# Kernel optimization log

Measured on AMD Instinct MI355X. Metric: run time of the kernel, lower is better.

The kernel has to match this reference:

```python
import jax, jax.numpy as jnp
import numpy as np

B, T, D = 4, 2048, 1024
H, HD = 16, 64  # num_heads, head_size; H*HD == D
DFF = 4 * D
EPS = 1e-5

def _ln(x, g, b):
    mu = jnp.mean(x, axis=-1, keepdims=True)
    var = jnp.mean(jnp.square(x - mu), axis=-1, keepdims=True)
    return (x - mu) * jax.lax.rsqrt(var + EPS) * g + b

def setup_inputs() -> dict:
    key = jax.random.key(0)
    ks = jax.random.split(key, 12)
    s = lambda fan_in: 1.0 / np.sqrt(fan_in)
    return {
        "x": jax.random.normal(ks[0], (B, T, D), jnp.float32),
        "Wq": jax.random.normal(ks[1], (H, D, HD), jnp.float32) * s(D),
        "Wk": jax.random.normal(ks[2], (H, D, HD), jnp.float32) * s(D),
        "Wv": jax.random.normal(ks[3], (H, D, HD), jnp.float32) * s(D),
        "Wo": jax.random.normal(ks[4], (D, D), jnp.float32) * s(D),
        "bo": jax.random.normal(ks[5], (D,), jnp.float32) * 0.01,
        "W1": jax.random.normal(ks[6], (D, DFF), jnp.float32) * s(D),
        "b1": jax.random.normal(ks[7], (DFF,), jnp.float32) * 0.01,
        "W2": jax.random.normal(ks[8], (DFF, D), jnp.float32) * s(DFF),
        "b2": jax.random.normal(ks[9], (D,), jnp.float32) * 0.01,
        "g1": jnp.ones((D,), jnp.float32),
        "be1": jnp.zeros((D,), jnp.float32),
        "g2": jnp.ones((D,), jnp.float32),
        "be2": jnp.zeros((D,), jnp.float32),
    }

def reference(x, Wq, Wk, Wv, Wo, bo, W1, b1, W2, b2, g1, be1, g2, be2):
    # pre-LN attention
    h = _ln(x, g1, be1)                                   # [B,T,D]
    q = jnp.einsum('btd,hde->bhte', h, Wq)                # [B,H,T,HD]
    k = jnp.einsum('btd,hde->bhte', h, Wk)
    v = jnp.einsum('btd,hde->bhte', h, Wv)
    scores = jnp.einsum('bhte,bhse->bhts', q, k) * (HD ** -0.5)  # [B,H,T,T]
    mask = jnp.tril(jnp.ones((T, T), bool))
    scores = jnp.where(mask, scores, -jnp.inf)
    attn = jax.nn.softmax(scores, axis=-1)
    ctx = jnp.einsum('bhts,bhse->bhte', attn, v)          # [B,H,T,HD]
    ctx = ctx.transpose(0, 2, 1, 3).reshape(B, T, D)      # concat heads
    x = x + jnp.einsum('btd,de->bte', ctx, Wo) + bo
    # pre-LN FFN
    h2 = _ln(x, g2, be2)
    ff = jax.nn.relu(jnp.einsum('btd,df->btf', h2, W1) + b1)
    x = x + jnp.einsum('btf,fd->btd', ff, W2) + b2
    return x
```

## Files before the change

kernel.cpp:

```cpp
#include <hip/hip_runtime.h>
#include <stdint.h>

#define B_ 4
#define T_ 2048
#define D_ 1024
#define H_ 16
#define HD_ 64
#define DFF_ 4096
#define M_ (B_ * T_)

typedef __bf16 bf16x8 __attribute__((ext_vector_type(8)));
typedef float f32x4 __attribute__((ext_vector_type(4)));

__device__ __forceinline__ uint16_t f2bf(float f) {
  union { float f; uint32_t u; } v;
  v.f = f;
  uint32_t r = v.u + 0x7FFF + ((v.u >> 16) & 1);
  return (uint16_t)(r >> 16);
}

#define GLD_LDS(gp, lp)                                                        \
  __builtin_amdgcn_global_load_lds(                                            \
      (const __attribute__((address_space(1))) void*)(gp),                     \
      (__attribute__((address_space(3))) void*)(lp), 16, 0, 0)

__global__ __launch_bounds__(256) void ln_bf16(const float* __restrict__ x,
                                               const float* __restrict__ gamma,
                                               const float* __restrict__ beta,
                                               uint16_t* __restrict__ out) {
  __shared__ float red[4];
  const int tid = threadIdx.x;
  const size_t row = blockIdx.x;
  const float4 v = ((const float4*)(x + row * D_))[tid];
  float s = v.x + v.y + v.z + v.w;
#pragma unroll
  for (int off = 32; off >= 1; off >>= 1) s += __shfl_xor(s, off, 64);
  if ((tid & 63) == 0) red[tid >> 6] = s;
  __syncthreads();
  const float mean = (red[0] + red[1] + red[2] + red[3]) * (1.0f / D_);
  const float d0 = v.x - mean, d1 = v.y - mean, d2 = v.z - mean, d3 = v.w - mean;
  float ss = d0 * d0 + d1 * d1 + d2 * d2 + d3 * d3;
#pragma unroll
  for (int off = 32; off >= 1; off >>= 1) ss += __shfl_xor(ss, off, 64);
  __syncthreads();
  if ((tid & 63) == 0) red[tid >> 6] = ss;
  __syncthreads();
  const float var = (red[0] + red[1] + red[2] + red[3]) * (1.0f / D_);
  const float rstd = rsqrtf(var + 1e-5f);
  const float4 g = ((const float4*)gamma)[tid];
  const float4 b = ((const float4*)beta)[tid];
  ushort4 o;
  o.x = f2bf(d0 * rstd * g.x + b.x);
  o.y = f2bf(d1 * rstd * g.y + b.y);
  o.z = f2bf(d2 * rstd * g.z + b.z);
  o.w = f2bf(d3 * rstd * g.w + b.w);
  ((ushort4*)(out + row * D_))[tid] = o;
}

__global__ __launch_bounds__(256) void transpose_cast(const float* __restrict__ in,
                                                      uint16_t* __restrict__ out,
                                                      int R, int C) {
  __shared__ float tile[32][33];
  const int tx = threadIdx.x & 31, ty = threadIdx.x >> 5;
  const int c0 = blockIdx.x * 32, r0 = blockIdx.y * 32;
#pragma unroll
  for (int i = 0; i < 32; i += 8)
    tile[ty + i][tx] = in[(size_t)(r0 + ty + i) * C + c0 + tx];
  __syncthreads();
#pragma unroll
  for (int i = 0; i < 32; i += 8)
    out[(size_t)(c0 + ty + i) * R + r0 + tx] = f2bf(tile[tx][ty + i]);
}

__global__ __launch_bounds__(256) void qkv_wt(const float* __restrict__ Wq,
                                              const float* __restrict__ Wk,
                                              const float* __restrict__ Wv,
                                              uint16_t* __restrict__ out) {
  __shared__ float tile[32][33];
  const int tx = threadIdx.x & 31, ty = threadIdx.x >> 5;
  const int z = blockIdx.z, which = z >> 4, hh = z & 15;
  const float* W = (which == 0) ? Wq : ((which == 1) ? Wk : Wv);
  const float* in = W + (size_t)hh * D_ * HD_;
  const int e0 = blockIdx.x * 32, d0 = blockIdx.y * 32;
#pragma unroll
  for (int i = 0; i < 32; i += 8)
    tile[ty + i][tx] = in[(size_t)(d0 + ty + i) * HD_ + e0 + tx];
  __syncthreads();
#pragma unroll
  for (int i = 0; i < 32; i += 8)
    out[((size_t)(which * 1024 + hh * 64) + e0 + ty + i) * D_ + d0 + tx] =
        f2bf(tile[tx][ty + i]);
}

__global__ __launch_bounds__(256) void gemm_bf16(const uint16_t* __restrict__ A,
                                                 const uint16_t* __restrict__ Bt,
                                                 void* __restrict__ C,
                                                 const float* __restrict__ bias,
                                                 const float* __restrict__ resid,
                                                 int M, int N, int K, int flags) {
  __shared__ __align__(16) uint16_t As[128 * 32];
  __shared__ __align__(16) uint16_t Bs[128 * 32];
  const int tid = threadIdx.x;
  const int lane = tid & 63, w = tid >> 6;
  const int quad = lane >> 4, lr = lane & 15;
  const int wr = w >> 1, wc = w & 1;
  const int bn0 = blockIdx.x * 128, bm0 = blockIdx.y * 128;

  f32x4 acc[4][4];
#pragma unroll
  for (int i = 0; i < 4; i++)
#pragma unroll
    for (int j = 0; j < 4; j++) acc[i][j] = f32x4{0.f, 0.f, 0.f, 0.f};

  const int s_sub = lane >> 2, s_slot = lane & 3;

  for (int k0 = 0; k0 < K; k0 += 32) {
#pragma unroll
    for (int i = 0; i < 2; i++) {
      const int r = w * 32 + i * 16 + s_sub;
      const int cg = s_slot ^ ((r >> 1) & 3);
      GLD_LDS(A + (size_t)(bm0 + r) * K + k0 + cg * 8, As + (w * 32 + i * 16) * 32);
      GLD_LDS(Bt + (size_t)(bn0 + r) * K + k0 + cg * 8, Bs + (w * 32 + i * 16) * 32);
    }
    __syncthreads();

    bf16x8 af[4], bfr[4];
#pragma unroll
    for (int i = 0; i < 4; i++) {
      const int m = wr * 64 + i * 16 + lr;
      const int slot = quad ^ ((m >> 1) & 3);
      af[i] = *(const bf16x8*)(As + m * 32 + slot * 8);
    }
#pragma unroll
    for (int j = 0; j < 4; j++) {
      const int n = wc * 64 + j * 16 + lr;
      const int slot = quad ^ ((n >> 1) & 3);
      bfr[j] = *(const bf16x8*)(Bs + n * 32 + slot * 8);
    }
#pragma unroll
    for (int i = 0; i < 4; i++)
#pragma unroll
      for (int j = 0; j < 4; j++)
        acc[i][j] = __builtin_amdgcn_mfma_f32_16x16x32_bf16(af[i], bfr[j], acc[i][j], 0, 0, 0);
    __syncthreads();
  }

  const int base_m = bm0 + wr * 64 + quad * 4;
  const int base_n = bn0 + wc * 64 + lr;
#pragma unroll
  for (int i = 0; i < 4; i++) {
#pragma unroll
    for (int j = 0; j < 4; j++) {
      const int col = base_n + j * 16;
      const float bv = bias ? bias[col] : 0.f;
#pragma unroll
      for (int r = 0; r < 4; r++) {
        const size_t row = base_m + i * 16 + r;
        float v = acc[i][j][r] + bv;
        if (resid) v += resid[row * N + col];
        if (flags & 1) v = fmaxf(v, 0.f);
        if (flags & 2)
          ((uint16_t*)C)[row * N + col] = f2bf(v);
        else
          ((float*)C)[row * N + col] = v;
      }
    }
  }
}

__global__ __launch_bounds__(256) void v_transpose(const uint16_t* __restrict__ qkv,
                                                   uint16_t* __restrict__ vtb) {
  __shared__ __align__(16) uint16_t tile[64 * 72];
  const int tid = threadIdx.x;
  const int t0 = blockIdx.x * 64;
  const int bh = blockIdx.y;
  const int b = bh >> 4, h = bh & 15;
  const uint16_t* src = qkv + (size_t)b * T_ * 3072 + 2048 + h * 64;
#pragma unroll
  for (int u = 0; u < 2; u++) {
    const int uu = tid + u * 256;
    const int r = uu >> 3, c = uu & 7;
    *(int4*)(tile + r * 72 + c * 8) =
        *(const int4*)(src + (size_t)(t0 + r) * 3072 + c * 8);
  }
  __syncthreads();
  uint16_t* dst = vtb + ((size_t)bh * 64) * T_ + t0;
#pragma unroll
  for (int u = 0; u < 2; u++) {
    const int uu = tid + u * 256;
    const int e = uu >> 3, c2 = uu & 7;
    union { uint16_t u16[8]; int4 v; } tmp;
#pragma unroll
    for (int jj = 0; jj < 8; jj++) tmp.u16[jj] = tile[(c2 * 8 + jj) * 72 + e];
    *(int4*)(dst + (size_t)e * T_ + c2 * 8) = tmp.v;
  }
}

__global__ __launch_bounds__(256) void attn_mfma(const uint16_t* __restrict__ qkv,
                                                 const uint16_t* __restrict__ vtb,
                                                 uint16_t* __restrict__ ctx) {
  __shared__ __align__(16) uint16_t Ks[64 * 72];
  __shared__ __align__(16) uint16_t Vt[64 * 72];
  __shared__ __align__(16) uint16_t Ps[128 * 72];
  const int tid = threadIdx.x;
  const int lane = tid & 63, w = tid >> 6;
  const int quad = lane >> 4, lr = lane & 15;
  const int h = blockIdx.y, b = blockIdx.z;
  const uint16_t* base = qkv + (size_t)b * T_ * 3072 + h * 64;
  const uint16_t* vbase = vtb + ((size_t)(b * H_ + h) * 64) * T_;
  const int sr = tid >> 3, sc = tid & 7;

#pragma unroll
  for (int half = 0; half < 2; half++) {
    const int tq = (half == 0) ? (int)blockIdx.x : 15 - (int)blockIdx.x;
    const int q0 = tq * 128;

    bf16x8 aq[2][2];
#pragma unroll
    for (int i = 0; i < 2; i++)
#pragma unroll
      for (int ks = 0; ks < 2; ks++)
        aq[i][ks] = *(const bf16x8*)(base + (size_t)(q0 + w * 32 + i * 16 + lr) * 3072 +
                                     ks * 32 + quad * 8);

    f32x4 oacc[2][4];
#pragma unroll
    for (int i = 0; i < 2; i++)
#pragma unroll
      for (int j = 0; j < 4; j++) oacc[i][j] = f32x4{0.f, 0.f, 0.f, 0.f};
    float l_part[2] = {0.f, 0.f};

    const int row_min_w = q0 + w * 32;
    const int row_max_w = row_min_w + 31;
    const int nt = 2 * tq + 2;

    for (int st = 0; st < nt; st++) {
      __syncthreads();
#pragma unroll
      for (int u = 0; u < 2; u++) {
        const int r = sr + u * 32;
        *(int4*)(Ks + r * 72 + sc * 8) =
            *(const int4*)(base + 1024 + (size_t)(st * 64 + r) * 3072 + sc * 8);
        *(int4*)(Vt + r * 72 + sc * 8) =
            *(const int4*)(vbase + (size_t)r * T_ + st * 64 + sc * 8);
      }
      __syncthreads();

      if (st * 64 > row_max_w) continue;

      f32x4 sa[2][4];
#pragma unroll
      for (int i = 0; i < 2; i++)
#pragma unroll
        for (int sf = 0; sf < 4; sf++) sa[i][sf] = f32x4{0.f, 0.f, 0.f, 0.f};
#pragma unroll
      for (int ks = 0; ks < 2; ks++) {
        bf16x8 ak[4];
#pragma unroll
        for (int sf = 0; sf < 4; sf++)
          ak[sf] = *(const bf16x8*)(Ks + (sf * 16 + lr) * 72 + ks * 32 + quad * 8);
#pragma unroll
        for (int i = 0; i < 2; i++)
#pragma unroll
          for (int sf = 0; sf < 4; sf++)
            sa[i][sf] = __builtin_amdgcn_mfma_f32_16x16x32_bf16(ak[sf], aq[i][ks],
                                                                sa[i][sf], 0, 0, 0);
      }

#pragma unroll
      for (int i = 0; i < 2; i++) {
        const int mrow = q0 + w * 32 + i * 16 + lr;
#pragma unroll
        for (int sf = 0; sf < 4; sf++) {
          const int s0 = st * 64 + sf * 16 + quad * 4;
          float p[4];
#pragma unroll
          for (int r = 0; r < 4; r++) {
            float sv = sa[i][sf][r];
            if (s0 + r > mrow) sv = -1e30f;
            p[r] = exp2f(fmaf(sv, 0.18033688f, -28.8539008f));
            l_part[i] += p[r];
          }
          ushort4 pk;
          pk.x = f2bf(p[0]);
          pk.y = f2bf(p[1]);
          pk.z = f2bf(p[2]);
          pk.w = f2bf(p[3]);
          *(ushort4*)(Ps + (size_t)(w * 32 + i * 16 + lr) * 72 + sf * 16 + quad * 4) = pk;
        }
      }

#pragma unroll
      for (int ks = 0; ks < 2; ks++) {
        bf16x8 ap[2], bv[4];
#pragma unroll
        for (int i = 0; i < 2; i++)
          ap[i] = *(const bf16x8*)(Ps + (size_t)(w * 32 + i * 16 + lr) * 72 + ks * 32 +
                                   quad * 8);
#pragma unroll
        for (int j = 0; j < 4; j++)
          bv[j] = *(const bf16x8*)(Vt + (j * 16 + lr) * 72 + ks * 32 + quad * 8);
#pragma unroll
        for (int i = 0; i < 2; i++)
#pragma unroll
          for (int j = 0; j < 4; j++)
            oacc[i][j] =
                __builtin_amdgcn_mfma_f32_16x16x32_bf16(ap[i], bv[j], oacc[i][j], 0, 0, 0);
      }
    }

    float linv[2];
#pragma unroll
    for (int i = 0; i < 2; i++) {
      float l = l_part[i];
      l += __shfl_xor(l, 16, 64);
      l += __shfl_xor(l, 32, 64);
      linv[i] = 1.f / l;
    }
    uint16_t* ob =
        ctx + ((size_t)b * T_ + q0 + w * 32 + quad * 4) * D_ + h * 64 + lr;
#pragma unroll
    for (int i = 0; i < 2; i++)
#pragma unroll
      for (int r = 0; r < 4; r++) {
        const float inv = __shfl(linv[i], quad * 4 + r, 64);
#pragma unroll
        for (int j = 0; j < 4; j++)
          ob[(size_t)(i * 16 + r) * D_ + j * 16] = f2bf(oacc[i][j][r] * inv);
      }
  }
}

extern "C" void kernel_launch(void* const* d_in, const int* in_sizes, int n_in,
                              void* d_out, int out_size, void* d_ws, size_t ws_size,
                              hipStream_t stream) {
  const float* x = (const float*)d_in[0];
  const float* Wq = (const float*)d_in[1];
  const float* Wk = (const float*)d_in[2];
  const float* Wv = (const float*)d_in[3];
  const float* Wo = (const float*)d_in[4];
  const float* bo = (const float*)d_in[5];
  const float* W1 = (const float*)d_in[6];
  const float* b1 = (const float*)d_in[7];
  const float* W2 = (const float*)d_in[8];
  const float* b2 = (const float*)d_in[9];
  const float* g1 = (const float*)d_in[10];
  const float* be1 = (const float*)d_in[11];
  const float* g2 = (const float*)d_in[12];
  const float* be2 = (const float*)d_in[13];
  float* out = (float*)d_out;

  const size_t MB = 1024ull * 1024ull;
  if (ws_size < 200 * MB) return;
  char* ws = (char*)d_ws;
  uint16_t* hbuf = (uint16_t*)(ws + 0 * MB);
  uint16_t* wqkvt = (uint16_t*)(ws + 16 * MB);
  uint16_t* wot = (uint16_t*)(ws + 22 * MB);
  uint16_t* w1t = (uint16_t*)(ws + 24 * MB);
  uint16_t* w2t = (uint16_t*)(ws + 32 * MB);
  float* x1 = (float*)(ws + 40 * MB);
  uint16_t* qkvb = (uint16_t*)(ws + 72 * MB);
  uint16_t* ctxb = (uint16_t*)(ws + 120 * MB);
  uint16_t* vtb = (uint16_t*)(ws + 136 * MB);
  uint16_t* ffb = (uint16_t*)(ws + 136 * MB);

  qkv_wt<<<dim3(2, 32, 48), 256, 0, stream>>>(Wq, Wk, Wv, wqkvt);
  transpose_cast<<<dim3(32, 32), 256, 0, stream>>>(Wo, wot, 1024, 1024);
  transpose_cast<<<dim3(128, 32), 256, 0, stream>>>(W1, w1t, 1024, 4096);
  transpose_cast<<<dim3(32, 128), 256, 0, stream>>>(W2, w2t, 4096, 1024);

  ln_bf16<<<M_, 256, 0, stream>>>(x, g1, be1, hbuf);
  gemm_bf16<<<dim3(24, 64), 256, 0, stream>>>(hbuf, wqkvt, qkvb, nullptr, nullptr,
                                              M_, 3 * D_, D_, 2);
  v_transpose<<<dim3(T_ / 64, B_ * H_), 256, 0, stream>>>(qkvb, vtb);
  attn_mfma<<<dim3(8, H_, B_), 256, 0, stream>>>(qkvb, vtb, ctxb);
  gemm_bf16<<<dim3(8, 64), 256, 0, stream>>>(ctxb, wot, x1, bo, x, M_, D_, D_, 0);
  ln_bf16<<<M_, 256, 0, stream>>>(x1, g2, be2, hbuf);
  gemm_bf16<<<dim3(32, 64), 256, 0, stream>>>(hbuf, w1t, ffb, b1, nullptr, M_, DFF_,
                                              D_, 1 | 2);
  gemm_bf16<<<dim3(8, 64), 256, 0, stream>>>(ffb, w2t, out, b2, x1, M_, D_, DFF_, 0);
}
```

Before: 629.2 us.

## Add grouped tile rasterization to GEMM and split-K the FFN2 projection

The GEMM now takes a 1D grid and maps block ids so that groups of 16 M-tiles sweep across N, aiming to improve L2 reuse of weight and activation tiles. Explicit leading dimensions are added so the second FFN GEMM can be split along K into two half-GEMMs writing fp32 partials. A new elementwise kernel sums the partials with the bias and residual. The split adds extra partial-sum memory traffic and a launch, and the two halves still run one after the other.

```diff
diff --git a/kernel.cpp b/kernel.cpp
--- a/kernel.cpp
+++ b/kernel.cpp
@@ -97,14 +97,23 @@
                                                  void* __restrict__ C,
                                                  const float* __restrict__ bias,
                                                  const float* __restrict__ resid,
-                                                 int M, int N, int K, int flags) {
+                                                 int M, int N, int K, int lda,
+                                                 int ldb, int flags) {
   __shared__ __align__(16) uint16_t As[128 * 32];
   __shared__ __align__(16) uint16_t Bs[128 * 32];
   const int tid = threadIdx.x;
   const int lane = tid & 63, w = tid >> 6;
   const int quad = lane >> 4, lr = lane & 15;
   const int wr = w >> 1, wc = w & 1;
-  const int bn0 = blockIdx.x * 128, bm0 = blockIdx.y * 128;
+
+  const int n_tiles = N >> 7;
+  const int pid = blockIdx.x;
+  const int grp = 16 * n_tiles;
+  const int gid = pid / grp;
+  const int rem = pid - gid * grp;
+  const int nt = rem / 16;
+  const int mt = gid * 16 + (rem - nt * 16);
+  const int bn0 = nt * 128, bm0 = mt * 128;
 
   f32x4 acc[4][4];
 #pragma unroll
@@ -119,8 +128,8 @@
     for (int i = 0; i < 2; i++) {
       const int r = w * 32 + i * 16 + s_sub;
       const int cg = s_slot ^ ((r >> 1) & 3);
-      GLD_LDS(A + (size_t)(bm0 + r) * K + k0 + cg * 8, As + (w * 32 + i * 16) * 32);
-      GLD_LDS(Bt + (size_t)(bn0 + r) * K + k0 + cg * 8, Bs + (w * 32 + i * 16) * 32);
+      GLD_LDS(A + (size_t)(bm0 + r) * lda + k0 + cg * 8, As + (w * 32 + i * 16) * 32);
+      GLD_LDS(Bt + (size_t)(bn0 + r) * ldb + k0 + cg * 8, Bs + (w * 32 + i * 16) * 32);
     }
     __syncthreads();
 
@@ -166,6 +175,24 @@
       }
     }
   }
+}
+
+__global__ __launch_bounds__(256) void ffn2_combine(const float* __restrict__ p0,
+                                                    const float* __restrict__ p1,
+                                                    const float* __restrict__ x1,
+                                                    const float* __restrict__ b2,
+                                                    float* __restrict__ out) {
+  const int i = blockIdx.x * 256 + threadIdx.x;
+  const float4 a = ((const float4*)p0)[i];
+  const float4 b = ((const float4*)p1)[i];
+  const float4 r = ((const float4*)x1)[i];
+  const float4 bb = ((const float4*)b2)[i & 255];
+  float4 o;
+  o.x = a.x + b.x + r.x + bb.x;
+  o.y = a.y + b.y + r.y + bb.y;
+  o.z = a.z + b.z + r.z + bb.z;
+  o.w = a.w + b.w + r.w + bb.w;
+  ((float4*)out)[i] = o;
 }
 
 __global__ __launch_bounds__(256) void v_transpose(const uint16_t* __restrict__ qkv,
@@ -363,6 +390,8 @@
   uint16_t* ctxb = (uint16_t*)(ws + 120 * MB);
   uint16_t* vtb = (uint16_t*)(ws + 136 * MB);
   uint16_t* ffb = (uint16_t*)(ws + 136 * MB);
+  float* p0 = (float*)(ws + 72 * MB);
+  float* p1 = (float*)(ws + 104 * MB);
 
   qkv_wt<<<dim3(2, 32, 48), 256, 0, stream>>>(Wq, Wk, Wv, wqkvt);
   transpose_cast<<<dim3(32, 32), 256, 0, stream>>>(Wo, wot, 1024, 1024);
@@ -370,13 +399,17 @@
   transpose_cast<<<dim3(32, 128), 256, 0, stream>>>(W2, w2t, 4096, 1024);
 
   ln_bf16<<<M_, 256, 0, stream>>>(x, g1, be1, hbuf);
-  gemm_bf16<<<dim3(24, 64), 256, 0, stream>>>(hbuf, wqkvt, qkvb, nullptr, nullptr,
-                                              M_, 3 * D_, D_, 2);
+  gemm_bf16<<<64 * 24, 256, 0, stream>>>(hbuf, wqkvt, qkvb, nullptr, nullptr, M_,
+                                         3 * D_, D_, D_, D_, 2);
   v_transpose<<<dim3(T_ / 64, B_ * H_), 256, 0, stream>>>(qkvb, vtb);
   attn_mfma<<<dim3(8, H_, B_), 256, 0, stream>>>(qkvb, vtb, ctxb);
-  gemm_bf16<<<dim3(8, 64), 256, 0, stream>>>(ctxb, wot, x1, bo, x, M_, D_, D_, 0);
+  gemm_bf16<<<64 * 8, 256, 0, stream>>>(ctxb, wot, x1, bo, x, M_, D_, D_, D_, D_, 0);
   ln_bf16<<<M_, 256, 0, stream>>>(x1, g2, be2, hbuf);
-  gemm_bf16<<<dim3(32, 64), 256, 0, stream>>>(hbuf, w1t, ffb, b1, nullptr, M_, DFF_,
-                                              D_, 1 | 2);
-  gemm_bf16<<<dim3(8, 64), 256, 0, stream>>>(ffb, w2t, out, b2, x1, M_, D_, DFF_, 0);
-}
+  gemm_bf16<<<64 * 32, 256, 0, stream>>>(hbuf, w1t, ffb, b1, nullptr, M_, DFF_, D_,
+                                         D_, D_, 1 | 2);
+  gemm_bf16<<<64 * 8, 256, 0, stream>>>(ffb, w2t, p0, nullptr, nullptr, M_, D_,
+                                        DFF_ / 2, DFF_, DFF_, 0);
+  gemm_bf16<<<64 * 8, 256, 0, stream>>>(ffb + DFF_ / 2, w2t + DFF_ / 2, p1, nullptr,
+                                        nullptr, M_, D_, DFF_ / 2, DFF_, DFF_, 0);
+  ffn2_combine<<<(M_ * D_ / 4) / 256, 256, 0, stream>>>(p0, p1, x1, b2, out);
+}
```

Result: faster. 609.6 us (-3.1%).
